# Performance work log

Measured on AMD Instinct MI355X. Metric: run time of the kernel, lower is better.

Reference implementation:

```python
import jax, jax.numpy as jnp
import numpy as np
from jax import lax

BLANK_ID = 0
NEG_INF = -1e10  # finite stand-in for log(0); module uses LOG_0 = -1e10

B, T, H, V, L = 32, 1000, 512, 2048, 100


def setup_inputs() -> dict:
    key = jax.random.key(0)
    k1, k2, k3, k4, k5, k6 = jax.random.split(key, 6)
    eouts = jax.random.normal(k1, (B, T, H), dtype=jnp.float32)
    W = jax.random.normal(k2, (V, H), dtype=jnp.float32) * (1.0 / np.sqrt(H))
    b = jax.random.normal(k3, (V,), dtype=jnp.float32) * 0.01
    ys = jax.random.randint(k4, (B, L), 1, V, dtype=jnp.int32)  # labels exclude blank=0
    ylens = jax.random.randint(k5, (B,), L // 2, L + 1, dtype=jnp.int32)
    # ensure T_b >= 2*L_b + 1 so every alignment is feasible
    elens = jnp.clip(jax.random.randint(k6, (B,), T // 2, T + 1, dtype=jnp.int32), 2 * L + 1, T)
    return {"eouts": eouts, "W": W, "b": b, "ys": ys, "elens": elens, "ylens": ylens}


def ctc_loss_sum(log_probs, ys, elens, ylens):
    """Batched CTC forward DP. log_probs: [B,T,V]; ys: [B,L]; returns sum loss."""
    Bb, Tt, Vv = log_probs.shape
    Ll = ys.shape[1]
    S = 2 * Ll + 1
    # extended label sequence: blank, y1, blank, y2, ..., blank
    ext = jnp.zeros((Bb, S), dtype=jnp.int32).at[:, 1::2].set(ys)
    # gather per-frame log-probs of extended labels: [B,T,S]
    lp_ext = jnp.take_along_axis(log_probs, jnp.broadcast_to(ext[:, None, :], (Bb, Tt, S)), axis=2)
    # s-2 skip allowed iff ext[s] != blank and ext[s] != ext[s-2]
    ext_m2 = jnp.pad(ext, ((0, 0), (2, 0)), constant_values=-1)[:, :S]
    skip_ok = (ext != BLANK_ID) & (ext != ext_m2)
    valid = jnp.arange(S)[None, :] < (2 * ylens[:, None] + 1)  # [B,S]

    a0 = jnp.full((Bb, S), NEG_INF, dtype=log_probs.dtype)
    a0 = a0.at[:, 0].set(lp_ext[:, 0, 0]).at[:, 1].set(lp_ext[:, 0, 1])
    a0 = jnp.where(valid, a0, NEG_INF)

    def step(a, lp_t):  # a: [B,S], lp_t: [B,S]
        a1 = a
        a2 = jnp.pad(a, ((0, 0), (1, 0)), constant_values=NEG_INF)[:, :S]
        a3 = jnp.where(skip_ok, jnp.pad(a, ((0, 0), (2, 0)), constant_values=NEG_INF)[:, :S], NEG_INF)
        new = jnp.logaddexp(jnp.logaddexp(a1, a2), a3) + lp_t
        new = jnp.where(valid, new, NEG_INF)
        return new, new

    _, alphas_rest = lax.scan(step, a0, jnp.swapaxes(lp_ext, 0, 1)[1:])  # [T-1,B,S]
    alphas = jnp.concatenate([a0[None], alphas_rest], axis=0)  # [T,B,S]

    a_final = alphas[elens - 1, jnp.arange(Bb)]  # [B,S]
    last = jnp.take_along_axis(a_final, (2 * ylens)[:, None], axis=1)[:, 0]
    prev = jnp.take_along_axis(a_final, (2 * ylens - 1)[:, None], axis=1)[:, 0]
    loss_b = -jnp.logaddexp(last, prev)
    # zero_infinity=True: replace non-finite (numerically huge) losses with 0
    loss_b = jnp.where(loss_b < -0.5 * NEG_INF, loss_b, 0.0)
    return jnp.sum(loss_b)


def reference(eouts, W, b, ys, elens, ylens):
    logits = jnp.einsum("bth,vh->btv", eouts, W) + b  # self.output(eouts)
    log_probs = jax.nn.log_softmax(logits, axis=-1)
    loss_ctc = ctc_loss_sum(log_probs, ys, elens, ylens) / eouts.shape[0]
    return loss_ctc
```

## Files before the change

kernel.cpp:

```cpp
#include <hip/hip_runtime.h>
#include <hip/hip_bf16.h>

#define B_ 32
#define T_ 1000
#define H_ 512
#define V_ 2048
#define L_ 100
#define M_ (B_*T_)
#define GSTRIDE 104
#define LOG2E 1.4426950408889634f
#define LSE_SHIFT 48.0f
#define BIAS60 1.152921504606847e18f

typedef __attribute__((ext_vector_type(8))) short bf16x8;
typedef __attribute__((ext_vector_type(4))) float f32x4;

#define AS_G(p)  ((const __attribute__((address_space(1))) unsigned int*)(p))
#define AS_L(p)  ((__attribute__((address_space(3))) unsigned int*)(p))

__device__ __forceinline__ unsigned short f2bf(float x) {
    unsigned int u; __builtin_memcpy(&u, &x, 4);
    unsigned int r = (u + 0x7fffu + ((u >> 16) & 1u)) >> 16;
    return (unsigned short)r;
}

__device__ __forceinline__ float dpp_shr1(float x) {
    int r = __builtin_amdgcn_update_dpp(0, __builtin_bit_cast(int, x), 0x138, 0xf, 0xf, false);
    return __builtin_bit_cast(float, r);
}
template<int CTRL>
__device__ __forceinline__ float fmax_dpp(float x) {
    int s = __builtin_amdgcn_update_dpp(0, __builtin_bit_cast(int, x), CTRL, 0xf, 0xf, false);
    return fmaxf(x, __builtin_bit_cast(float, s));
}
__device__ __forceinline__ float wave_max_nonneg(float x) {
    x = fmax_dpp<0x111>(x);
    x = fmax_dpp<0x112>(x);
    x = fmax_dpp<0x114>(x);
    x = fmax_dpp<0x118>(x);
    x = fmax_dpp<0x142>(x);
    x = fmax_dpp<0x143>(x);
    return __builtin_bit_cast(float, __builtin_amdgcn_readlane(__builtin_bit_cast(int, x), 63));
}
template<int CTRL>
__device__ __forceinline__ float fadd_dpp(float x) {
    int s = __builtin_amdgcn_update_dpp(0, __builtin_bit_cast(int, x), CTRL, 0xf, 0xf, false);
    return x + __builtin_bit_cast(float, s);
}
__device__ __forceinline__ float rowsum16(float x) {
    x = fadd_dpp<0x111>(x);
    x = fadd_dpp<0x112>(x);
    x = fadd_dpp<0x114>(x);
    x = fadd_dpp<0x118>(x);
    return x;
}

__global__ __launch_bounds__(256) void prep_kernel(
        const float* __restrict__ eouts, const float* __restrict__ W,
        unsigned short* __restrict__ eb, unsigned short* __restrict__ wb,
        float* __restrict__ Srow, float* __restrict__ out)
{
    const int E4 = M_*H_/4;
    const int W4 = V_*H_/4;
    const int S4 = M_/4;
    int idx = blockIdx.x*256 + threadIdx.x;
    if (idx == 0) out[0] = 0.f;
    if (idx < E4) {
        float4 v = ((const float4*)eouts)[idx];
        ushort4 o; o.x=f2bf(v.x); o.y=f2bf(v.y); o.z=f2bf(v.z); o.w=f2bf(v.w);
        ((ushort4*)eb)[idx] = o;
    } else if (idx < E4 + W4) {
        int j = idx - E4;
        float4 v = ((const float4*)W)[j];
        ushort4 o; o.x=f2bf(v.x); o.y=f2bf(v.y); o.z=f2bf(v.z); o.w=f2bf(v.w);
        ((ushort4*)wb)[j] = o;
    } else if (idx < E4 + W4 + S4) {
        int j = idx - E4 - W4;
        ((float4*)Srow)[j] = make_float4(0.f,0.f,0.f,0.f);
    }
}

__global__ __launch_bounds__(512, 1) void gemm_lse_kernel(
        const unsigned short* __restrict__ eb, const unsigned short* __restrict__ wb,
        const float* __restrict__ bias, float* __restrict__ Srow)
{
    __shared__ __align__(16) unsigned short Ab[2][256*64];
    __shared__ __align__(16) unsigned short Bb[2][256*64];
    __shared__ float rs[256];
    const int tid  = threadIdx.x;
    const int w    = tid >> 6;
    const int lane = tid & 63;
    const int m    = lane & 15;
    const int qh   = lane >> 4;
    const int wr   = w >> 2;
    const int wc   = w & 3;
    const int rl   = m & 7;
    const int lrow = lane >> 3;
    const int k8   = ((lane & 7) ^ lrow) * 8;
    const int lin   = blockIdx.x;
    const int ytile = lin & 31;
    const int nbase = (lin >> 5) * 256;
    const int ntiles = (124 - ytile)/32 + 1;
    int mb_cur = ytile * 256;

    if (tid < 256) rs[tid] = 0.f;

    float bv[4];
    #pragma unroll
    for (int ni=0;ni<4;ni++) bv[ni] = bias[nbase + wc*64 + ni*16 + m];

    f32x4 acc[8][4];
    #pragma unroll
    for (int i=0;i<8;i++)
        #pragma unroll
        for (int j=0;j<4;j++) acc[i][j] = (f32x4){0.f,0.f,0.f,0.f};
    bf16x8 af[2][2], bfr[4][2];

#define STAGE_A(sel, r, kt, mb) do { \
        const unsigned short* _s = eb + (size_t)((mb) + (r)*64 + w*8 + lrow)*H_ + (kt)*64 + k8; \
        __builtin_amdgcn_global_load_lds(AS_G(_s), AS_L(&Ab[sel][((r)*64 + w*8)*64]), 16, 0, 0); \
    } while(0)
#define STAGE_B(sel, r, kt) do { \
        const unsigned short* _s = wb + (size_t)(nbase + (r)*64 + w*8 + lrow)*H_ + (kt)*64 + k8; \
        __builtin_amdgcn_global_load_lds(AS_G(_s), AS_L(&Bb[sel][((r)*64 + w*8)*64]), 16, 0, 0); \
    } while(0)

#define LOADB(sel) \
    _Pragma("unroll") \
    for (int ni=0; ni<4; ++ni) { \
        const int brow = wc*64 + ni*16 + m; \
        bfr[ni][0] = *(const bf16x8*)(&Bb[sel][brow*64 + ((qh ^ rl))*8]); \
        bfr[ni][1] = *(const bf16x8*)(&Bb[sel][brow*64 + (((4+qh) ^ rl))*8]); \
    }
#define LOADA(sel, qq) \
    _Pragma("unroll") \
    for (int mi2=0; mi2<2; ++mi2) { \
        const int arow = wr*128 + ((qq)*2+mi2)*16 + m; \
        af[mi2][0] = *(const bf16x8*)(&Ab[sel][arow*64 + ((qh ^ rl))*8]); \
        af[mi2][1] = *(const bf16x8*)(&Ab[sel][arow*64 + (((4+qh) ^ rl))*8]); \
    }
#define MFMA16(qq) \
    __builtin_amdgcn_s_setprio(1); \
    _Pragma("unroll") \
    for (int mi2=0; mi2<2; ++mi2) \
        _Pragma("unroll") \
        for (int ni=0; ni<4; ++ni) { \
            acc[(qq)*2+mi2][ni] = __builtin_amdgcn_mfma_f32_16x16x32_bf16(af[mi2][0], bfr[ni][0], acc[(qq)*2+mi2][ni], 0, 0, 0); \
            acc[(qq)*2+mi2][ni] = __builtin_amdgcn_mfma_f32_16x16x32_bf16(af[mi2][1], bfr[ni][1], acc[(qq)*2+mi2][ni], 0, 0, 0); \
        } \
    __builtin_amdgcn_s_setprio(0);
#define BARX() __builtin_amdgcn_s_barrier()
#define WAIT_LGKM() do { asm volatile("s_waitcnt lgkmcnt(0)" ::: "memory"); \
                         __builtin_amdgcn_sched_barrier(0); } while(0)

    STAGE_B(0,0,0); STAGE_B(0,1,0);
    STAGE_B(0,2,0); STAGE_B(0,3,0);
    STAGE_A(0,1,0,mb_cur); STAGE_A(0,3,0,mb_cur);
    STAGE_A(0,0,0,mb_cur); STAGE_A(0,2,0,mb_cur);
    STAGE_B(1,0,1); STAGE_B(1,1,1);
    STAGE_B(1,2,1); STAGE_B(1,3,1);
    STAGE_A(1,1,1,mb_cur); STAGE_A(1,3,1,mb_cur);
    asm volatile("s_waitcnt vmcnt(6)" ::: "memory");
    BARX();

    #pragma unroll 1
    for (int mt = 0; mt < ntiles; ++mt) {
        const int mb_nxt = (ytile + 32*(mt+1)) * 256;
        #pragma unroll 1
        for (int it = 0; it < 4; ++it) {
            const bool last = (mt == ntiles-1) && (it == 3);
            const int k1 = 2*it + 1;
            const int k2 = (2*it + 2) & 7;
            const int k3 = (2*it + 3) & 7;
            const int mbs = (it < 3) ? mb_cur : mb_nxt;
            LOADB(0) LOADA(0,3)
            STAGE_A(1,0,k1,mb_cur); STAGE_A(1,2,k1,mb_cur);
            BARX(); WAIT_LGKM();
            MFMA16(3)
            BARX();
            LOADA(0,2)
            if (!last) { STAGE_B(0,0,k2); STAGE_B(0,1,k2); }
            BARX(); WAIT_LGKM();
            MFMA16(2)
            BARX();
            LOADA(0,1)
            if (!last) { STAGE_B(0,2,k2); STAGE_B(0,3,k2); }
            BARX(); WAIT_LGKM();
            MFMA16(1)
            BARX();
            LOADA(0,0)
            if (!last) { STAGE_A(0,1,k2,mbs); STAGE_A(0,3,k2,mbs); }
            BARX(); WAIT_LGKM();
            MFMA16(0)
            if (!last) { asm volatile("s_waitcnt vmcnt(6)" ::: "memory"); }
            else       { asm volatile("s_waitcnt vmcnt(0)" ::: "memory"); }
            BARX();
            LOADB(1) LOADA(1,3)
            if (!last) { STAGE_A(0,0,k2,mbs); STAGE_A(0,2,k2,mbs); }
            BARX(); WAIT_LGKM();
            MFMA16(3)
            BARX();
            LOADA(1,2)
            if (!last) { STAGE_B(1,0,k3); STAGE_B(1,1,k3); }
            BARX(); WAIT_LGKM();
            MFMA16(2)
            BARX();
            LOADA(1,1)
            if (!last) { STAGE_B(1,2,k3); STAGE_B(1,3,k3); }
            BARX(); WAIT_LGKM();
            MFMA16(1)
            BARX();
            LOADA(1,0)
            if (!last) { STAGE_A(1,1,k3,mbs); STAGE_A(1,3,k3,mbs); }
            BARX(); WAIT_LGKM();
            MFMA16(0)
            if (!last) { asm volatile("s_waitcnt vmcnt(6)" ::: "memory"); }
            else       { asm volatile("s_waitcnt vmcnt(0)" ::: "memory"); }
            BARX();
        }

        {
            #pragma unroll
            for (int mi=0;mi<8;mi++) {
                #pragma unroll
                for (int r=0;r<4;r++) {
                    float s = 0.f;
                    #pragma unroll
                    for (int ni=0;ni<4;ni++)
                        s += exp2f((acc[mi][ni][r] + bv[ni]) * LOG2E - LSE_SHIFT);
                    s = rowsum16(s);
                    if (m == 15) atomicAdd(&rs[wr*128 + mi*16 + qh*4 + r], s);
                }
            }
            WAIT_LGKM();
            BARX();
            if (tid < 256) {
                atomicAdd(&Srow[mb_cur + tid], rs[tid]);
                rs[tid] = 0.f;
            }
            #pragma unroll
            for (int i=0;i<8;i++)
                #pragma unroll
                for (int j=0;j<4;j++) acc[i][j] = (f32x4){0.f,0.f,0.f,0.f};
        }
        mb_cur = mb_nxt;
    }
#undef STAGE_A
#undef STAGE_B
#undef LOADB
#undef LOADA
#undef MFMA16
#undef BARX
#undef WAIT_LGKM
}

__global__ __launch_bounds__(256) void gather_mfma_kernel(
        const unsigned short* __restrict__ eb, const unsigned short* __restrict__ wb,
        const float* __restrict__ bias, const int* __restrict__ ys,
        const float* __restrict__ Srow, float* __restrict__ g)
{
    __shared__ __align__(16) unsigned short As[128*64];
    __shared__ __align__(16) unsigned short Bs[128*64];
    __shared__ float ls[128];
    const int tid  = threadIdx.x;
    const int w    = tid >> 6;
    const int lane = tid & 63;
    const int m    = lane & 15;
    const int q    = lane >> 4;
    const int wrow = w >> 1;
    const int wcol = w & 1;
    const int b    = blockIdx.y;
    const int tb   = blockIdx.x * 128;

    if (tid < 128) {
        int t = tb + tid;
        ls[tid] = (t < T_) ? (LSE_SHIFT + log2f(Srow[b*T_ + t])) : 0.f;
    }

    const int rbase = w*32 + (lane >> 3);
    const int k8    = (((lane & 7) ^ ((lane >> 3) & 7)) * 8);
    const int rl    = m & 7;

    int vrow[4];
    #pragma unroll
    for (int j=0;j<4;++j) {
        int labr = rbase + j*8;
        vrow[j] = (labr == 0 || labr > L_) ? 0 : ys[b*L_ + labr - 1];
    }
    int labc[4]; float bv[4];
    #pragma unroll
    for (int ni=0;ni<4;++ni) {
        int lab = wcol*64 + ni*16 + m;
        labc[ni] = lab;
        int v = (lab == 0 || lab > L_) ? 0 : ys[b*L_ + lab - 1];
        bv[ni] = bias[v];
    }

    f32x4 acc[4][4];
    #pragma unroll
    for (int i=0;i<4;i++)
        #pragma unroll
        for (int j=0;j<4;j++) acc[i][j] = (f32x4){0.f,0.f,0.f,0.f};

    for (int kc = 0; kc < 8; ++kc) {
        __syncthreads();
        #pragma unroll
        for (int j = 0; j < 4; ++j) {
            const unsigned short* ga = eb + (size_t)(b*T_ + tb + rbase + j*8)*H_ + kc*64 + k8;
            __builtin_amdgcn_global_load_lds(AS_G(ga), AS_L(As + (w*4+j)*512), 16, 0, 0);
            const unsigned short* gw = wb + (size_t)vrow[j]*H_ + kc*64 + k8;
            __builtin_amdgcn_global_load_lds(AS_G(gw), AS_L(Bs + (w*4+j)*512), 16, 0, 0);
        }
        __syncthreads();
        #pragma unroll
        for (int kk = 0; kk < 2; ++kk) {
            const int sw = ((kk*4 + q) ^ rl) * 8;
            bf16x8 af[4], bfr[4];
            #pragma unroll
            for (int mi=0;mi<4;mi++)
                af[mi] = *(const bf16x8*)(As + (wrow*8 + mi*2 + (m>>3))*512 + rl*64 + sw);
            #pragma unroll
            for (int ni=0;ni<4;ni++)
                bfr[ni] = *(const bf16x8*)(Bs + (wcol*8 + ni*2 + (m>>3))*512 + rl*64 + sw);
            #pragma unroll
            for (int mi=0;mi<4;mi++)
                #pragma unroll
                for (int ni=0;ni<4;ni++)
                    acc[mi][ni] = __builtin_amdgcn_mfma_f32_16x16x32_bf16(
                        af[mi], bfr[ni], acc[mi][ni], 0, 0, 0);
        }
    }

    #pragma unroll
    for (int mi=0;mi<4;mi++) {
        #pragma unroll
        for (int r=0;r<4;r++) {
            int trow = wrow*64 + mi*16 + q*4 + r;
            int t = tb + trow;
            float l2 = ls[trow];
            #pragma unroll
            for (int ni=0;ni<4;ni++) {
                if (t < T_ && labc[ni] <= L_) {
                    float p = exp2f((acc[mi][ni][r] + bv[ni]) * LOG2E - l2);
                    int off = (labc[ni] == 0) ? 0 : labc[ni] + 1;
                    g[(size_t)(b*T_ + t)*GSTRIDE + off] = p;
                }
            }
        }
    }
}

__global__ __launch_bounds__(128, 1) void ctc_dp_kernel(
        const float* __restrict__ g, const int* __restrict__ ys,
        const int* __restrict__ elens, const int* __restrict__ ylens,
        float* __restrict__ out)
{
    __shared__ __align__(16) float ring[2*2048];
    const int b    = blockIdx.x;
    const int tid  = threadIdx.x;
    const int wv   = tid >> 6;
    const int lane = tid & 63;
    const float* gb = g + (size_t)b * T_ * GSTRIDE;
    const int ylen = ylens[b];
    const int elen = elens[b];
    const int kmax = (elen - 1) >> 4;

    const int Sv   = 2*ylen + 1;
    const int s0   = 4*lane;
    const float msk0 = (s0   < Sv) ? 1.f : 0.f;
    const float msk1 = (s0+1 < Sv) ? 1.f : 0.f;
    const float msk2 = (s0+2 < Sv) ? 1.f : 0.f;
    const float msk3 = (s0+3 < Sv) ? 1.f : 0.f;
    const int l0 = 2*lane, l1 = 2*lane + 1;
    int i0 = min(max(l0,1), L_-1);
    int i1 = min(l1, L_-1);
    const float sk1 = (l0 >= 1 && l0 < L_ && ys[b*L_+i0] != ys[b*L_+i0-1]) ? 1.f : 0.f;
    const float sk3 = (l1 < L_        && ys[b*L_+i1] != ys[b*L_+i1-1]) ? 1.f : 0.f;

    float a0 = 0.f, a1 = 0.f, a2 = 0.f, a3 = 0.f, C2 = 0.f;
    if (wv == 0) {
        a0 = (lane == 0) ? gb[0] : 0.f;
        a1 = (lane == 0) ? gb[2] : 0.f;
    } else {
        #pragma unroll
        for (int s = 0; s < 8; ++s) {
            int srow = min(2*s, T_-2);
            __builtin_amdgcn_global_load_lds(AS_G(gb + (size_t)srow*GSTRIDE + 4*lane),
                                             AS_L(ring + s*256), 16, 0, 0);
        }
    }

    auto dpstep = [&](float p0, float p1, float p2, float p3) {
        float um1 = dpp_shr1(a3);
        float n0 = a0 + um1;
        float n1 = a1 + a0 + sk1*um1;
        float n2 = a2 + a1;
        float n3 = a3 + a2 + sk3*a1;
        a0 = n0*p0; a1 = n1*p1; a2 = n2*p2; a3 = n3*p3;
    };
    auto renorm = [&]() {
        float mm = wave_max_nonneg(fmaxf(fmaxf(a0,a1), fmaxf(a2,a3)));
        if (mm > 0.f) {
            float rr = fminf(__fdividef(BIAS60, mm), 3.0e38f);
            C2 -= __log2f(rr);
            a0 *= rr; a1 *= rr; a2 *= rr; a3 *= rr;
        }
    };

    __syncthreads();

    for (int k = 0; k <= kmax; ++k) {
        if (wv == 1) {
            if (k < kmax) {
                float* dset = ring + ((k+1) & 1)*2048;
                int pbase = 8*(k + 1);
                #pragma unroll
                for (int s = 0; s < 8; ++s) {
                    int srow = min(2*(pbase + s), T_-2);
                    __builtin_amdgcn_global_load_lds(AS_G(gb + (size_t)srow*GSTRIDE + 4*lane),
                                                     AS_L(dset + s*256), 16, 0, 0);
                }
            }
        } else {
            const float* sb = ring + (k & 1)*2048;
            float P0[16], P1[16], P2[16], P3[16];
            #pragma unroll
            for (int s = 0; s < 8; ++s) {
                const float* slot = sb + s*256;
                float pb0 = slot[0];
                float pb1 = slot[104];
                float2 lo = *(const float2*)(slot + 2  + 2*lane);
                float2 hi = *(const float2*)(slot + 106 + 2*lane);
                P0[2*s]   = pb0*msk0; P1[2*s]   = lo.x*msk1;
                P2[2*s]   = pb0*msk2; P3[2*s]   = lo.y*msk3;
                P0[2*s+1] = pb1*msk0; P1[2*s+1] = hi.x*msk1;
                P2[2*s+1] = pb1*msk2; P3[2*s+1] = hi.y*msk3;
            }
            const int t0 = 16*k;
            #pragma unroll
            for (int j = 0; j < 16; ++j) {
                int t = t0 + j;
                if (t > 0 && t < elen)
                    dpstep(P0[j], P1[j], P2[j], P3[j]);
                if ((j & 7) == 7) renorm();
            }
        }
        __syncthreads();
    }

    if (wv == 0) {
        int sA = 2*ylen, sB = sA - 1;
        float vA = __shfl((sA & 2) ? a2 : a0, sA >> 2);
        float vB = __shfl((sB & 2) ? a3 : a1, sB >> 2);
        if (lane == 0) {
            float sum = vA + vB;
            float loss = 0.f;
            if (sum > 0.f) {
                loss = -(log2f(sum) + C2) * 0.6931471805599453f;
                if (!(loss < 5e9f)) loss = 0.f;
            }
            atomicAdd(out, loss * (1.0f/B_));
        }
    }
}

extern "C" void kernel_launch(void* const* d_in, const int* in_sizes, int n_in,
                              void* d_out, int out_size, void* d_ws, size_t ws_size,
                              hipStream_t stream)
{
    const float* eouts = (const float*)d_in[0];
    const float* W     = (const float*)d_in[1];
    const float* bias  = (const float*)d_in[2];
    const int*   ys    = (const int*)d_in[3];
    const int*   elens = (const int*)d_in[4];
    const int*   ylens = (const int*)d_in[5];
    float* out = (float*)d_out;

    char* ws = (char*)d_ws;
    unsigned short* eb = (unsigned short*)ws;
    unsigned short* wb = (unsigned short*)(ws + 32768000);
    float* Srow        = (float*)(ws + 34865152);
    float* g           = (float*)(ws + 34993152);

    prep_kernel<<<17057, 256, 0, stream>>>(eouts, W, eb, wb, Srow, out);
    gemm_lse_kernel<<<256, 512, 0, stream>>>(eb, wb, bias, Srow);
    gather_mfma_kernel<<<dim3(8, 32), 256, 0, stream>>>(eb, wb, bias, ys, Srow, g);
    ctc_dp_kernel<<<B_, 128, 0, stream>>>(g, ys, elens, ylens, out);
}
```

Baseline: 265.4 us.

## Replace LDS producer-wave ring in CTC DP with register double-buffered prefetch

```diff
diff --git a/kernel.cpp b/kernel.cpp
--- a/kernel.cpp
+++ b/kernel.cpp
@@ -350,16 +350,13 @@
     }
 }
 
-__global__ __launch_bounds__(128, 1) void ctc_dp_kernel(
+__global__ __launch_bounds__(64, 1) void ctc_dp_kernel(
         const float* __restrict__ g, const int* __restrict__ ys,
         const int* __restrict__ elens, const int* __restrict__ ylens,
         float* __restrict__ out)
 {
-    __shared__ __align__(16) float ring[2*2048];
     const int b    = blockIdx.x;
-    const int tid  = threadIdx.x;
-    const int wv   = tid >> 6;
-    const int lane = tid & 63;
+    const int lane = threadIdx.x & 63;
     const float* gb = g + (size_t)b * T_ * GSTRIDE;
     const int ylen = ylens[b];
     const int elen = elens[b];
@@ -377,18 +374,12 @@
     const float sk1 = (l0 >= 1 && l0 < L_ && ys[b*L_+i0] != ys[b*L_+i0-1]) ? 1.f : 0.f;
     const float sk3 = (l1 < L_        && ys[b*L_+i1] != ys[b*L_+i1-1]) ? 1.f : 0.f;
 
-    float a0 = 0.f, a1 = 0.f, a2 = 0.f, a3 = 0.f, C2 = 0.f;
-    if (wv == 0) {
-        a0 = (lane == 0) ? gb[0] : 0.f;
-        a1 = (lane == 0) ? gb[2] : 0.f;
-    } else {
-        #pragma unroll
-        for (int s = 0; s < 8; ++s) {
-            int srow = min(2*s, T_-2);
-            __builtin_amdgcn_global_load_lds(AS_G(gb + (size_t)srow*GSTRIDE + 4*lane),
-                                             AS_L(ring + s*256), 16, 0, 0);
-        }
-    }
+    const int cl  = min(lane, 49);
+    const int blj = lane & 15;
+
+    float a0 = (lane == 0) ? gb[0] : 0.f;
+    float a1 = (lane == 0) ? gb[2] : 0.f;
+    float a2 = 0.f, a3 = 0.f, C2 = 0.f;
 
     auto dpstep = [&](float p0, float p1, float p2, float p3) {
         float um1 = dpp_shr1(a3);
@@ -407,60 +398,54 @@
         }
     };
 
-    __syncthreads();
-
-    for (int k = 0; k <= kmax; ++k) {
-        if (wv == 1) {
-            if (k < kmax) {
-                float* dset = ring + ((k+1) & 1)*2048;
-                int pbase = 8*(k + 1);
-                #pragma unroll
-                for (int s = 0; s < 8; ++s) {
-                    int srow = min(2*(pbase + s), T_-2);
-                    __builtin_amdgcn_global_load_lds(AS_G(gb + (size_t)srow*GSTRIDE + 4*lane),
-                                                     AS_L(dset + s*256), 16, 0, 0);
-                }
-            }
-        } else {
-            const float* sb = ring + (k & 1)*2048;
-            float P0[16], P1[16], P2[16], P3[16];
-            #pragma unroll
-            for (int s = 0; s < 8; ++s) {
-                const float* slot = sb + s*256;
-                float pb0 = slot[0];
-                float pb1 = slot[104];
-                float2 lo = *(const float2*)(slot + 2  + 2*lane);
-                float2 hi = *(const float2*)(slot + 106 + 2*lane);
-                P0[2*s]   = pb0*msk0; P1[2*s]   = lo.x*msk1;
-                P2[2*s]   = pb0*msk2; P3[2*s]   = lo.y*msk3;
-                P0[2*s+1] = pb1*msk0; P1[2*s+1] = hi.x*msk1;
-                P2[2*s+1] = pb1*msk2; P3[2*s+1] = hi.y*msk3;
-            }
-            const int t0 = 16*k;
-            #pragma unroll
-            for (int j = 0; j < 16; ++j) {
-                int t = t0 + j;
-                if (t > 0 && t < elen)
-                    dpstep(P0[j], P1[j], P2[j], P3[j]);
-                if ((j & 7) == 7) renorm();
-            }
-        }
-        __syncthreads();
-    }
-
-    if (wv == 0) {
-        int sA = 2*ylen, sB = sA - 1;
-        float vA = __shfl((sA & 2) ? a2 : a0, sA >> 2);
-        float vB = __shfl((sB & 2) ? a3 : a1, sB >> 2);
-        if (lane == 0) {
-            float sum = vA + vB;
-            float loss = 0.f;
-            if (sum > 0.f) {
-                loss = -(log2f(sum) + C2) * 0.6931471805599453f;
-                if (!(loss < 5e9f)) loss = 0.f;
-            }
-            atomicAdd(out, loss * (1.0f/B_));
-        }
+    float2 PA[16], PB[16];
+    float  blA, blB;
+
+#define LOADSET(PX, BLX, kb) do { \
+        const int _t0 = 16*(kb); \
+        BLX = gb[(size_t)min(_t0 + blj, T_-1) * GSTRIDE]; \
+        _Pragma("unroll") \
+        for (int j = 0; j < 16; ++j) \
+            PX[j] = *(const float2*)(gb + (size_t)min(_t0 + j, T_-1) * GSTRIDE + 2 + 2*cl); \
+    } while(0)
+
+#define COMPSET(PX, BLX, kb) do { \
+        const int _t0 = 16*(kb); \
+        _Pragma("unroll") \
+        for (int j = 0; j < 16; ++j) { \
+            float _bl = __builtin_bit_cast(float, \
+                __builtin_amdgcn_readlane(__builtin_bit_cast(int, BLX), j)); \
+            int _t = _t0 + j; \
+            if (_t > 0 && _t < elen) \
+                dpstep(_bl*msk0, PX[j].x*msk1, _bl*msk2, PX[j].y*msk3); \
+            if ((j & 7) == 7) renorm(); \
+        } \
+    } while(0)
+
+    LOADSET(PA, blA, 0);
+    #pragma unroll 1
+    for (int kk = 0; kk <= kmax; kk += 2) {
+        if (kk + 1 <= kmax) LOADSET(PB, blB, kk + 1);
+        COMPSET(PA, blA, kk);
+        if (kk + 1 <= kmax) {
+            if (kk + 2 <= kmax) LOADSET(PA, blA, kk + 2);
+            COMPSET(PB, blB, kk + 1);
+        }
+    }
+#undef LOADSET
+#undef COMPSET
+
+    int sA = 2*ylen, sB = sA - 1;
+    float vA = __shfl((sA & 2) ? a2 : a0, sA >> 2);
+    float vB = __shfl((sB & 2) ? a3 : a1, sB >> 2);
+    if (lane == 0) {
+        float sum = vA + vB;
+        float loss = 0.f;
+        if (sum > 0.f) {
+            loss = -(log2f(sum) + C2) * 0.6931471805599453f;
+            if (!(loss < 5e9f)) loss = 0.f;
+        }
+        atomicAdd(out, loss * (1.0f/B_));
     }
 }
 
@@ -485,5 +470,5 @@
     prep_kernel<<<17057, 256, 0, stream>>>(eouts, W, eb, wb, Srow, out);
     gemm_lse_kernel<<<256, 512, 0, stream>>>(eb, wb, bias, Srow);
     gather_mfma_kernel<<<dim3(8, 32), 256, 0, stream>>>(eb, wb, bias, ys, Srow, g);
-    ctc_dp_kernel<<<B_, 128, 0, stream>>>(g, ys, elens, ylens, out);
-}
+    ctc_dp_kernel<<<B_, 64, 0, stream>>>(g, ys, elens, ylens, out);
+}
```

Measured after the change: 272.8 us. +2.8%, slower.

## Halve GEMM inner-loop phases with larger A fragment batches per barrier

Applied to the files above, without the earlier changes.

```diff
diff --git a/kernel.cpp b/kernel.cpp
--- a/kernel.cpp
+++ b/kernel.cpp
@@ -114,7 +114,7 @@
     for (int i=0;i<8;i++)
         #pragma unroll
         for (int j=0;j<4;j++) acc[i][j] = (f32x4){0.f,0.f,0.f,0.f};
-    bf16x8 af[2][2], bfr[4][2];
+    bf16x8 af2[4][2], bfr[4][2];
 
 #define STAGE_A(sel, r, kt, mb) do { \
         const unsigned short* _s = eb + (size_t)((mb) + (r)*64 + w*8 + lrow)*H_ + (kt)*64 + k8; \
@@ -132,26 +132,28 @@
         bfr[ni][0] = *(const bf16x8*)(&Bb[sel][brow*64 + ((qh ^ rl))*8]); \
         bfr[ni][1] = *(const bf16x8*)(&Bb[sel][brow*64 + (((4+qh) ^ rl))*8]); \
     }
-#define LOADA(sel, qq) \
+#define LOADA2(sel, qlo) \
     _Pragma("unroll") \
-    for (int mi2=0; mi2<2; ++mi2) { \
-        const int arow = wr*128 + ((qq)*2+mi2)*16 + m; \
-        af[mi2][0] = *(const bf16x8*)(&Ab[sel][arow*64 + ((qh ^ rl))*8]); \
-        af[mi2][1] = *(const bf16x8*)(&Ab[sel][arow*64 + (((4+qh) ^ rl))*8]); \
-    }
-#define MFMA16(qq) \
+    for (int a=0; a<4; ++a) { \
+        const int arow = wr*128 + ((qlo)*2+a)*16 + m; \
+        af2[a][0] = *(const bf16x8*)(&Ab[sel][arow*64 + ((qh ^ rl))*8]); \
+        af2[a][1] = *(const bf16x8*)(&Ab[sel][arow*64 + (((4+qh) ^ rl))*8]); \
+    }
+#define MFMA32(qlo) \
     __builtin_amdgcn_s_setprio(1); \
     _Pragma("unroll") \
-    for (int mi2=0; mi2<2; ++mi2) \
+    for (int a=0; a<4; ++a) \
         _Pragma("unroll") \
         for (int ni=0; ni<4; ++ni) { \
-            acc[(qq)*2+mi2][ni] = __builtin_amdgcn_mfma_f32_16x16x32_bf16(af[mi2][0], bfr[ni][0], acc[(qq)*2+mi2][ni], 0, 0, 0); \
-            acc[(qq)*2+mi2][ni] = __builtin_amdgcn_mfma_f32_16x16x32_bf16(af[mi2][1], bfr[ni][1], acc[(qq)*2+mi2][ni], 0, 0, 0); \
+            acc[(qlo)*2+a][ni] = __builtin_amdgcn_mfma_f32_16x16x32_bf16(af2[a][0], bfr[ni][0], acc[(qlo)*2+a][ni], 0, 0, 0); \
+            acc[(qlo)*2+a][ni] = __builtin_amdgcn_mfma_f32_16x16x32_bf16(af2[a][1], bfr[ni][1], acc[(qlo)*2+a][ni], 0, 0, 0); \
         } \
     __builtin_amdgcn_s_setprio(0);
 #define BARX() __builtin_amdgcn_s_barrier()
 #define WAIT_LGKM() do { asm volatile("s_waitcnt lgkmcnt(0)" ::: "memory"); \
                          __builtin_amdgcn_sched_barrier(0); } while(0)
+#define VMC8()  asm volatile("s_waitcnt vmcnt(8)" ::: "memory")
+#define VMC0()  asm volatile("s_waitcnt vmcnt(0)" ::: "memory")
 
     STAGE_B(0,0,0); STAGE_B(0,1,0);
     STAGE_B(0,2,0); STAGE_B(0,3,0);
@@ -160,7 +162,7 @@
     STAGE_B(1,0,1); STAGE_B(1,1,1);
     STAGE_B(1,2,1); STAGE_B(1,3,1);
     STAGE_A(1,1,1,mb_cur); STAGE_A(1,3,1,mb_cur);
-    asm volatile("s_waitcnt vmcnt(6)" ::: "memory");
+    VMC8();
     BARX();
 
     #pragma unroll 1
@@ -173,49 +175,37 @@
             const int k2 = (2*it + 2) & 7;
             const int k3 = (2*it + 3) & 7;
             const int mbs = (it < 3) ? mb_cur : mb_nxt;
-            LOADB(0) LOADA(0,3)
+            LOADB(0) LOADA2(0,2)
             STAGE_A(1,0,k1,mb_cur); STAGE_A(1,2,k1,mb_cur);
             BARX(); WAIT_LGKM();
-            MFMA16(3)
+            MFMA32(2)
+            VMC8();
             BARX();
-            LOADA(0,2)
-            if (!last) { STAGE_B(0,0,k2); STAGE_B(0,1,k2); }
+            LOADA2(0,0)
+            if (!last) {
+                STAGE_B(0,0,k2); STAGE_B(0,1,k2);
+                STAGE_B(0,2,k2); STAGE_B(0,3,k2);
+                STAGE_A(0,1,k2,mbs); STAGE_A(0,3,k2,mbs);
+            }
             BARX(); WAIT_LGKM();
-            MFMA16(2)
+            MFMA32(0)
+            if (!last) VMC8(); else VMC0();
             BARX();
-            LOADA(0,1)
-            if (!last) { STAGE_B(0,2,k2); STAGE_B(0,3,k2); }
-            BARX(); WAIT_LGKM();
-            MFMA16(1)
-            BARX();
-            LOADA(0,0)
-            if (!last) { STAGE_A(0,1,k2,mbs); STAGE_A(0,3,k2,mbs); }
-            BARX(); WAIT_LGKM();
-            MFMA16(0)
-            if (!last) { asm volatile("s_waitcnt vmcnt(6)" ::: "memory"); }
-            else       { asm volatile("s_waitcnt vmcnt(0)" ::: "memory"); }
-            BARX();
-            LOADB(1) LOADA(1,3)
+            LOADB(1) LOADA2(1,2)
             if (!last) { STAGE_A(0,0,k2,mbs); STAGE_A(0,2,k2,mbs); }
             BARX(); WAIT_LGKM();
-            MFMA16(3)
+            MFMA32(2)
+            if (!last) VMC8(); else VMC0();
             BARX();
-            LOADA(1,2)
-            if (!last) { STAGE_B(1,0,k3); STAGE_B(1,1,k3); }
+            LOADA2(1,0)
+            if (!last) {
+                STAGE_B(1,0,k3); STAGE_B(1,1,k3);
+                STAGE_B(1,2,k3); STAGE_B(1,3,k3);
+                STAGE_A(1,1,k3,mbs); STAGE_A(1,3,k3,mbs);
+            }
             BARX(); WAIT_LGKM();
-            MFMA16(2)
-            BARX();
-            LOADA(1,1)
-            if (!last) { STAGE_B(1,2,k3); STAGE_B(1,3,k3); }
-            BARX(); WAIT_LGKM();
-            MFMA16(1)
-            BARX();
-            LOADA(1,0)
-            if (!last) { STAGE_A(1,1,k3,mbs); STAGE_A(1,3,k3,mbs); }
-            BARX(); WAIT_LGKM();
-            MFMA16(0)
-            if (!last) { asm volatile("s_waitcnt vmcnt(6)" ::: "memory"); }
-            else       { asm volatile("s_waitcnt vmcnt(0)" ::: "memory"); }
+            MFMA32(0)
+            if (!last) VMC8(); else VMC0();
             BARX();
         }
 
@@ -248,10 +238,12 @@
 #undef STAGE_A
 #undef STAGE_B
 #undef LOADB
-#undef LOADA
-#undef MFMA16
+#undef LOADA2
+#undef MFMA32
 #undef BARX
 #undef WAIT_LGKM
+#undef VMC8
+#undef VMC0
 }
 
 __global__ __launch_bounds__(256) void gather_mfma_kernel(
```

After: 268.5 us. About the same (+1.2%).
